# Optimization experiments

Measured on AMD Instinct MI355X. Metric: run time of the kernel, lower is better.

Reference implementation:

```python
import jax, jax.numpy as jnp
import numpy as np

N_NODES = 200000
IN_SIZE = 128
OUT_SIZE = 128
N_EDGES = 600000


def setup_inputs() -> dict:
    key = jax.random.key(0)
    k1, k2, k3, k4 = jax.random.split(key, 4)
    embedding = jax.random.normal(k1, (N_NODES, IN_SIZE), dtype=jnp.float32)
    up2down_edge_index = jax.random.randint(k2, (2, N_EDGES), 0, N_NODES, dtype=jnp.int64)
    # GCNConv params (glorot weight, zero bias as in PyG defaults)
    scale = np.sqrt(6.0 / (IN_SIZE + OUT_SIZE)).astype(np.float32)
    W = jax.random.uniform(k3, (IN_SIZE, OUT_SIZE), dtype=jnp.float32, minval=-scale, maxval=scale)
    b = jnp.zeros((OUT_SIZE,), dtype=jnp.float32)
    return {"embedding": embedding, "up2down_edge_index": up2down_edge_index, "W": W, "b": b}


def reference(embedding, up2down_edge_index, W, b):
    # PyG GCNConv: add self-loops, symmetric normalization, linear transform,
    # scatter-sum aggregation, add bias.
    N = embedding.shape[0]
    loops = jnp.arange(N, dtype=up2down_edge_index.dtype)
    src = jnp.concatenate([up2down_edge_index[0], loops])  # message sources
    dst = jnp.concatenate([up2down_edge_index[1], loops])  # message targets

    # degree of each target node (edge_weight = 1)
    deg = jax.ops.segment_sum(jnp.ones_like(src, dtype=embedding.dtype), dst, num_segments=N)
    deg_inv_sqrt = jnp.where(deg > 0, jax.lax.rsqrt(jnp.maximum(deg, 1.0)), 0.0)
    norm = deg_inv_sqrt[src] * deg_inv_sqrt[dst]  # [E+N]

    h = embedding @ W  # [N, out]
    msg = h[src] * norm[:, None]  # gather + scale, [E+N, out]
    out = jax.ops.segment_sum(msg, dst, num_segments=N)  # scatter-add
    return out + b
```

## Files before the change

kernel.cpp:

```cpp
#include <hip/hip_runtime.h>
#include <hip/hip_bf16.h>
#include <stdint.h>

typedef __attribute__((ext_vector_type(8))) short short8v;
typedef __attribute__((ext_vector_type(4))) float f32x4;

__device__ __forceinline__ unsigned short f2bf(float f) {
  unsigned int u = __float_as_uint(f);
  u += 0x7fffu + ((u >> 16) & 1u);
  return (unsigned short)(u >> 16);
}
__device__ __forceinline__ float bf_lo(unsigned int v) { return __uint_as_float(v << 16); }
__device__ __forceinline__ float bf_hi(unsigned int v) { return __uint_as_float(v & 0xffff0000u); }

__global__ void k_count(const int* __restrict__ dst, int* deg, int E) {
  int e = blockIdx.x * blockDim.x + threadIdx.x;
  if (e < E) atomicAdd(&deg[dst[e]], 1);
}

__global__ void k_blocksum(const int* __restrict__ deg, int* partials, float* dis, int N) {
  __shared__ int s[256];
  int t = threadIdx.x;
  int i = blockIdx.x * 256 + t;
  int c = (i < N) ? deg[i] : 0;
  if (i < N) dis[i] = rsqrtf((float)(c + 1));
  s[t] = c;
  __syncthreads();
  for (int off = 128; off > 0; off >>= 1) {
    if (t < off) s[t] += s[t + off];
    __syncthreads();
  }
  if (t == 0) partials[blockIdx.x] = s[0];
}

__global__ void k_scan_partials(int* partials, int nb) {
  __shared__ int s[1024];
  int t = threadIdx.x;
  s[t] = (t < nb) ? partials[t] : 0;
  __syncthreads();
  for (int off = 1; off < 1024; off <<= 1) {
    int v = (t >= off) ? s[t - off] : 0;
    __syncthreads();
    s[t] += v;
    __syncthreads();
  }
  if (t < nb) partials[t] = (t == 0) ? 0 : s[t - 1];
}

__global__ void k_scan_final(const int* __restrict__ deg, const int* __restrict__ partials,
                             int* csr_off, int N, int E) {
  __shared__ int s[256];
  int t = threadIdx.x;
  int i = blockIdx.x * 256 + t;
  int c = (i < N) ? deg[i] : 0;
  s[t] = c;
  __syncthreads();
  for (int off = 1; off < 256; off <<= 1) {
    int v = (t >= off) ? s[t - off] : 0;
    __syncthreads();
    s[t] += v;
    __syncthreads();
  }
  if (i < N) csr_off[i] = partials[blockIdx.x] + s[t] - c;
  if (i == 0) csr_off[N] = E;
}

__global__ void k_fill(const int* __restrict__ src, const int* __restrict__ dst,
                       const int* __restrict__ csr_off, int* cursor, int* csr_src, int E) {
  int e = blockIdx.x * blockDim.x + threadIdx.x;
  if (e < E) {
    int d = dst[e];
    int p = atomicAdd(&cursor[d], 1);
    csr_src[csr_off[d] + p] = src[e];
  }
}

__global__ void k_wprep(const float* __restrict__ W, unsigned short* __restrict__ Wfrag) {
  int t = blockIdx.x * 256 + threadIdx.x;
  int j = t & 7;
  int lane = (t >> 3) & 63;
  int ktct = t >> 9;
  int kt = ktct & 3, ct = ktct >> 2;
  int col = ct * 16 + (lane & 15);
  int k = kt * 32 + 4 * (lane >> 4) + (j & 3) + 16 * (j >> 2);
  Wfrag[t] = f2bf(W[k * 128 + col]);
}

__device__ __forceinline__ short8v pack8(float4 a, float4 b) {
  short8v r;
  r[0] = (short)f2bf(a.x); r[1] = (short)f2bf(a.y);
  r[2] = (short)f2bf(a.z); r[3] = (short)f2bf(a.w);
  r[4] = (short)f2bf(b.x); r[5] = (short)f2bf(b.y);
  r[6] = (short)f2bf(b.z); r[7] = (short)f2bf(b.w);
  return r;
}

__global__ __launch_bounds__(256) void k_gemm2(const float* __restrict__ X,
     const unsigned short* __restrict__ Wfrag, const float* __restrict__ dis,
     unsigned short* __restrict__ hs, int N, int NCH, int nb) {
  __shared__ unsigned short Wl[16384];
  int t = threadIdx.x;
  for (int q = t; q < 2048; q += 256)
    ((uint4*)Wl)[q] = ((const uint4*)Wfrag)[q];
  __syncthreads();

  int wv = t >> 6, lane = t & 63;
  int lr = lane & 15, lg = lane >> 4;
  int c0 = (int)(((long long)blockIdx.x * NCH) / nb);
  int c1 = (int)(((long long)(blockIdx.x + 1) * NCH) / nb);

  for (int chunk = c0; chunk < c1; ++chunk) {
    int r0 = chunk * 64;
    int arow = r0 + wv * 16 + lr;
    short8v afr[4];
    if (r0 + 64 <= N) {
      const float* xp = X + (size_t)arow * 128 + 4 * lg;
      #pragma unroll
      for (int kt = 0; kt < 4; ++kt) {
        float4 v0 = *(const float4*)(xp + kt * 32);
        float4 v1 = *(const float4*)(xp + kt * 32 + 16);
        afr[kt] = pack8(v0, v1);
      }
    } else {
      #pragma unroll
      for (int kt = 0; kt < 4; ++kt) {
        float4 v0 = {0.f, 0.f, 0.f, 0.f}, v1 = {0.f, 0.f, 0.f, 0.f};
        if (arow < N) {
          const float* xp = X + (size_t)arow * 128 + 4 * lg;
          v0 = *(const float4*)(xp + kt * 32);
          v1 = *(const float4*)(xp + kt * 32 + 16);
        }
        afr[kt] = pack8(v0, v1);
      }
    }
    float dmul[4];
    #pragma unroll
    for (int r = 0; r < 4; ++r) {
      int row = r0 + wv * 16 + lg * 4 + r;
      dmul[r] = (row < N) ? dis[row] : 0.f;
    }
    #pragma unroll
    for (int ct = 0; ct < 8; ++ct) {
      f32x4 acc = {0.f, 0.f, 0.f, 0.f};
      #pragma unroll
      for (int kt = 0; kt < 4; ++kt) {
        short8v bfr = *(const short8v*)(Wl + (((ct * 4 + kt) * 64 + lane) * 8));
        acc = __builtin_amdgcn_mfma_f32_16x16x32_bf16(afr[kt], bfr, acc, 0, 0, 0);
      }
      int col = ct * 16 + lr;
      #pragma unroll
      for (int r = 0; r < 4; ++r) {
        int row = r0 + wv * 16 + lg * 4 + r;
        if (row < N) hs[(size_t)row * 128 + col] = f2bf(acc[r] * dmul[r]);
      }
    }
  }
}

__device__ __forceinline__ void acc8(float* a, uint4 g) {
  a[0] += bf_lo(g.x); a[1] += bf_hi(g.x);
  a[2] += bf_lo(g.y); a[3] += bf_hi(g.y);
  a[4] += bf_lo(g.z); a[5] += bf_hi(g.z);
  a[6] += bf_lo(g.w); a[7] += bf_hi(g.w);
}

__global__ __launch_bounds__(256) void k_agg2(const unsigned short* __restrict__ hs_,
     const int* __restrict__ csr_src, const int* __restrict__ csr_off,
     const float* __restrict__ dis, const float* __restrict__ bias,
     float* __restrict__ out, int N) {
  const uint4* hs = (const uint4*)hs_;
  int lane = threadIdx.x & 63;
  int c = lane & 15;
  int base = lane & 48;
  int gid = (blockIdx.x * blockDim.x + threadIdx.x) >> 4;
  int G = (gridDim.x * blockDim.x) >> 4;
  int i0 = (int)(((long long)gid * N) / G);
  int i1 = (int)(((long long)(gid + 1) * N) / G);
  if (i0 >= i1) return;
  float4 bA = ((const float4*)bias)[c * 2];
  float4 bB = ((const float4*)bias)[c * 2 + 1];
  int e1prev = csr_off[i0];
  for (int i = i0; i < i1; ++i) {
    int e0 = e1prev;
    int e1 = csr_off[i + 1];
    e1prev = e1;
    float a[8];
    uint4 sv = hs[(size_t)i * 16 + c];
    a[0] = bf_lo(sv.x); a[1] = bf_hi(sv.x);
    a[2] = bf_lo(sv.y); a[3] = bf_hi(sv.y);
    a[4] = bf_lo(sv.z); a[5] = bf_hi(sv.z);
    a[6] = bf_lo(sv.w); a[7] = bf_hi(sv.w);
    int e = e0;
    while (e < e1) {
      int p = e + c;
      int myidx = (p < e1) ? csr_src[p] : 0;
      int kb = (e1 - e < 16) ? (e1 - e) : 16;
      for (int k = 0; k < kb; k += 4) {
        int s0 = __shfl(myidx, base + k);
        int s1 = __shfl(myidx, base + k + 1);
        int s2 = __shfl(myidx, base + k + 2);
        int s3 = __shfl(myidx, base + k + 3);
        bool v1 = (k + 1 < kb), v2 = (k + 2 < kb), v3 = (k + 3 < kb);
        uint4 g0 = hs[(size_t)s0 * 16 + c];
        uint4 g1 = hs[(size_t)(v1 ? s1 : i) * 16 + c];
        uint4 g2 = hs[(size_t)(v2 ? s2 : i) * 16 + c];
        uint4 g3 = hs[(size_t)(v3 ? s3 : i) * 16 + c];
        if (!v1) { g1.x = g1.y = g1.z = g1.w = 0u; }
        if (!v2) { g2.x = g2.y = g2.z = g2.w = 0u; }
        if (!v3) { g3.x = g3.y = g3.z = g3.w = 0u; }
        acc8(a, g0); acc8(a, g1); acc8(a, g2); acc8(a, g3);
      }
      e += kb;
    }
    float di = dis[i];
    float4 o0, o1;
    o0.x = fmaf(di, a[0], bA.x); o0.y = fmaf(di, a[1], bA.y);
    o0.z = fmaf(di, a[2], bA.z); o0.w = fmaf(di, a[3], bA.w);
    o1.x = fmaf(di, a[4], bB.x); o1.y = fmaf(di, a[5], bB.y);
    o1.z = fmaf(di, a[6], bB.z); o1.w = fmaf(di, a[7], bB.w);
    float4* op = (float4*)(out + (size_t)i * 128);
    op[c * 2] = o0;
    op[c * 2 + 1] = o1;
  }
}

extern "C" void kernel_launch(void* const* d_in, const int* in_sizes, int n_in,
                              void* d_out, int out_size, void* d_ws, size_t ws_size,
                              hipStream_t stream) {
  const float* X    = (const float*)d_in[0];
  const int*   edge = (const int*)d_in[1];
  const float* W    = (const float*)d_in[2];
  const float* bias = (const float*)d_in[3];
  float* out = (float*)d_out;
  int N = in_sizes[0] / 128;
  int E = in_sizes[1] / 2;
  const int* srcArr = edge;
  const int* dstArr = edge + E;

  char* w = (char*)d_ws;
  auto align = [](size_t x) { return (x + 255) & ~(size_t)255; };
  size_t o = 0;
  int*   deg      = (int*)(w + o);   o += align((size_t)N * 4);
  int*   cursor   = (int*)(w + o);   o += align((size_t)N * 4);
  float* dis      = (float*)(w + o); o += align((size_t)N * 4);
  int*   csr_off  = (int*)(w + o);   o += align(((size_t)N + 1) * 4);
  int*   csr_src  = (int*)(w + o);   o += align((size_t)E * 4);
  int*   partials = (int*)(w + o);   o += align((size_t)4096 * 4);
  unsigned short* Wfrag = (unsigned short*)(w + o); o += align((size_t)16384 * 2);
  unsigned short* hs    = (unsigned short*)(w + o);

  int nbN = (N + 255) / 256;
  int nbE = (E + 255) / 256;
  int NCH = (N + 63) / 64;
  int nbG = 1024;

  hipMemsetAsync(deg, 0, align((size_t)N * 4) + (size_t)N * 4, stream);
  k_wprep<<<64, 256, 0, stream>>>(W, Wfrag);
  k_count<<<nbE, 256, 0, stream>>>(dstArr, deg, E);
  k_blocksum<<<nbN, 256, 0, stream>>>(deg, partials, dis, N);
  k_scan_partials<<<1, 1024, 0, stream>>>(partials, nbN);
  k_scan_final<<<nbN, 256, 0, stream>>>(deg, partials, csr_off, N, E);
  k_fill<<<nbE, 256, 0, stream>>>(srcArr, dstArr, csr_off, cursor, csr_src, E);
  k_gemm2<<<nbG, 256, 0, stream>>>(X, Wfrag, dis, hs, N, NCH, nbG);
  k_agg2<<<2048, 256, 0, stream>>>(hs, csr_src, csr_off, dis, bias, out, N);
}
```

Baseline: 179.4 us.

## Transpose GEMM MFMA operands for packed stores, one block per chunk, 8-wide gathers

The GEMM kernel swaps the MFMA A/B operands so each lane owns one row and four consecutive columns. That lets it write packed 8-byte bf16 stores instead of scattered 2-byte stores, and it needs only one dis load per lane. The persistent chunk loop is replaced by one block per 64-row chunk, which means more blocks, each reloading W into LDS. The aggregation inner loop gains an 8-wide unrolled gather path to put more loads in flight, at some register cost.

New measurement: 163.0 us. 1.1x faster.

```diff
diff --git a/kernel.cpp b/kernel.cpp
--- a/kernel.cpp
+++ b/kernel.cpp
@@ -9,6 +9,9 @@
   unsigned int u = __float_as_uint(f);
   u += 0x7fffu + ((u >> 16) & 1u);
   return (unsigned short)(u >> 16);
+}
+__device__ __forceinline__ unsigned int pack2bf(float a, float b) {
+  return (unsigned int)f2bf(a) | ((unsigned int)f2bf(b) << 16);
 }
 __device__ __forceinline__ float bf_lo(unsigned int v) { return __uint_as_float(v << 16); }
 __device__ __forceinline__ float bf_hi(unsigned int v) { return __uint_as_float(v & 0xffff0000u); }
@@ -95,64 +98,51 @@
   return r;
 }
 
-__global__ __launch_bounds__(256) void k_gemm2(const float* __restrict__ X,
+__global__ __launch_bounds__(256) void k_gemm3(const float* __restrict__ X,
      const unsigned short* __restrict__ Wfrag, const float* __restrict__ dis,
-     unsigned short* __restrict__ hs, int N, int NCH, int nb) {
+     unsigned short* __restrict__ hs, int N) {
   __shared__ unsigned short Wl[16384];
   int t = threadIdx.x;
-  for (int q = t; q < 2048; q += 256)
-    ((uint4*)Wl)[q] = ((const uint4*)Wfrag)[q];
+  #pragma unroll
+  for (int q = 0; q < 8; ++q)
+    ((uint4*)Wl)[q * 256 + t] = ((const uint4*)Wfrag)[q * 256 + t];
   __syncthreads();
 
   int wv = t >> 6, lane = t & 63;
   int lr = lane & 15, lg = lane >> 4;
-  int c0 = (int)(((long long)blockIdx.x * NCH) / nb);
-  int c1 = (int)(((long long)(blockIdx.x + 1) * NCH) / nb);
-
-  for (int chunk = c0; chunk < c1; ++chunk) {
-    int r0 = chunk * 64;
-    int arow = r0 + wv * 16 + lr;
-    short8v afr[4];
-    if (r0 + 64 <= N) {
-      const float* xp = X + (size_t)arow * 128 + 4 * lg;
-      #pragma unroll
-      for (int kt = 0; kt < 4; ++kt) {
-        float4 v0 = *(const float4*)(xp + kt * 32);
-        float4 v1 = *(const float4*)(xp + kt * 32 + 16);
-        afr[kt] = pack8(v0, v1);
-      }
-    } else {
-      #pragma unroll
-      for (int kt = 0; kt < 4; ++kt) {
-        float4 v0 = {0.f, 0.f, 0.f, 0.f}, v1 = {0.f, 0.f, 0.f, 0.f};
-        if (arow < N) {
-          const float* xp = X + (size_t)arow * 128 + 4 * lg;
-          v0 = *(const float4*)(xp + kt * 32);
-          v1 = *(const float4*)(xp + kt * 32 + 16);
-        }
-        afr[kt] = pack8(v0, v1);
-      }
-    }
-    float dmul[4];
+  int row = blockIdx.x * 64 + wv * 16 + lr;
+
+  short8v afr[4];
+  if (row < N) {
+    const float* xp = X + (size_t)row * 128 + 4 * lg;
     #pragma unroll
-    for (int r = 0; r < 4; ++r) {
-      int row = r0 + wv * 16 + lg * 4 + r;
-      dmul[r] = (row < N) ? dis[row] : 0.f;
-    }
+    for (int kt = 0; kt < 4; ++kt) {
+      float4 v0 = *(const float4*)(xp + kt * 32);
+      float4 v1 = *(const float4*)(xp + kt * 32 + 16);
+      afr[kt] = pack8(v0, v1);
+    }
+  } else {
     #pragma unroll
-    for (int ct = 0; ct < 8; ++ct) {
-      f32x4 acc = {0.f, 0.f, 0.f, 0.f};
-      #pragma unroll
-      for (int kt = 0; kt < 4; ++kt) {
-        short8v bfr = *(const short8v*)(Wl + (((ct * 4 + kt) * 64 + lane) * 8));
-        acc = __builtin_amdgcn_mfma_f32_16x16x32_bf16(afr[kt], bfr, acc, 0, 0, 0);
-      }
-      int col = ct * 16 + lr;
-      #pragma unroll
-      for (int r = 0; r < 4; ++r) {
-        int row = r0 + wv * 16 + lg * 4 + r;
-        if (row < N) hs[(size_t)row * 128 + col] = f2bf(acc[r] * dmul[r]);
-      }
+    for (int kt = 0; kt < 4; ++kt) {
+      float4 z = {0.f, 0.f, 0.f, 0.f};
+      afr[kt] = pack8(z, z);
+    }
+  }
+  float d = (row < N) ? dis[row] : 0.f;
+
+  #pragma unroll
+  for (int ct = 0; ct < 8; ++ct) {
+    f32x4 acc = {0.f, 0.f, 0.f, 0.f};
+    #pragma unroll
+    for (int kt = 0; kt < 4; ++kt) {
+      short8v wfr = *(const short8v*)(Wl + (((ct * 4 + kt) * 64 + lane) * 8));
+      acc = __builtin_amdgcn_mfma_f32_16x16x32_bf16(wfr, afr[kt], acc, 0, 0, 0);
+    }
+    if (row < N) {
+      uint2 uu;
+      uu.x = pack2bf(acc[0] * d, acc[1] * d);
+      uu.y = pack2bf(acc[2] * d, acc[3] * d);
+      *(uint2*)(hs + (size_t)row * 128 + ct * 16 + 4 * lg) = uu;
     }
   }
 }
@@ -195,7 +185,18 @@
       int p = e + c;
       int myidx = (p < e1) ? csr_src[p] : 0;
       int kb = (e1 - e < 16) ? (e1 - e) : 16;
-      for (int k = 0; k < kb; k += 4) {
+      int k = 0;
+      for (; k + 8 <= kb; k += 8) {
+        int s[8];
+        #pragma unroll
+        for (int q = 0; q < 8; ++q) s[q] = __shfl(myidx, base + k + q);
+        uint4 g[8];
+        #pragma unroll
+        for (int q = 0; q < 8; ++q) g[q] = hs[(size_t)s[q] * 16 + c];
+        #pragma unroll
+        for (int q = 0; q < 8; ++q) acc8(a, g[q]);
+      }
+      for (; k < kb; k += 4) {
         int s0 = __shfl(myidx, base + k);
         int s1 = __shfl(myidx, base + k + 1);
         int s2 = __shfl(myidx, base + k + 2);
@@ -251,8 +252,6 @@
 
   int nbN = (N + 255) / 256;
   int nbE = (E + 255) / 256;
-  int NCH = (N + 63) / 64;
-  int nbG = 1024;
 
   hipMemsetAsync(deg, 0, align((size_t)N * 4) + (size_t)N * 4, stream);
   k_wprep<<<64, 256, 0, stream>>>(W, Wfrag);
@@ -261,6 +260,6 @@
   k_scan_partials<<<1, 1024, 0, stream>>>(partials, nbN);
   k_scan_final<<<nbN, 256, 0, stream>>>(deg, partials, csr_off, N, E);
   k_fill<<<nbE, 256, 0, stream>>>(srcArr, dstArr, csr_off, cursor, csr_src, E);
-  k_gemm2<<<nbG, 256, 0, stream>>>(X, Wfrag, dis, hs, N, NCH, nbG);
+  k_gemm3<<<(N + 63) / 64, 256, 0, stream>>>(X, Wfrag, dis, hs, N);
   k_agg2<<<2048, 256, 0, stream>>>(hs, csr_src, csr_off, dis, bias, out, N);
 }
```
